# Kernel optimization log

Hardware: AMD Instinct MI355X
Metric: run time of the kernel (lower is better)

## Reference

```python
import jax, jax.numpy as jnp
import numpy as np

B, S, H = 4, 1024, 2560          # batch, seq, hidden_size
E, K, F = 32, 6, 1536            # num_experts, top_k, moe_intermediate_size
SHARED_F = 2 * 1536              # moe_num_shared_experts * moe_intermediate_size
NORM_MIN = 1e-12                 # config.moe_norm_min


def setup_inputs() -> dict:
    key = jax.random.key(0)
    ks = jax.random.split(key, 9)
    rnd = lambda k, shape, scale=0.02: jax.random.normal(k, shape, dtype=jnp.float32) * scale
    return {
        "hidden_states": jax.random.normal(ks[0], (B, S, H), dtype=jnp.float32),
        "router_w": rnd(ks[1], (E, H)),              # Ernie4_5_MoeTopKRouter.weight (fp32)
        "router_bias": jnp.zeros((E,), jnp.float32),  # moe_statics.e_score_correction_bias
        "gate_w": rnd(ks[2], (E, H, F)),
        "up_w": rnd(ks[3], (E, H, F)),
        "down_w": rnd(ks[4], (E, F, H)),
        "shared_gate_w": rnd(ks[5], (H, SHARED_F)),
        "shared_up_w": rnd(ks[6], (H, SHARED_F)),
        "shared_down_w": rnd(ks[7], (SHARED_F, H)),
    }


def _mlp(x, gw, uw, dw):
    # Ernie4_5_MoeMLP: down( silu(gate(x)) * up(x) ), no biases
    return (jax.nn.silu(x @ gw) * (x @ uw)) @ dw


def _forward(hidden_states, router_w, router_bias, gate_w, up_w, down_w,
             shared_gate_w, shared_up_w, shared_down_w):
    T = B * S
    xt = hidden_states.reshape(T, H)

    # shared experts path (always-on dense MLP)
    shared_out = _mlp(xt, shared_gate_w, shared_up_w, shared_down_w)

    # router: fp32 linear -> softmax -> (+ correction bias) -> top-k -> renorm
    logits = xt.astype(jnp.float32) @ router_w.T            # [T, E]
    probs = jax.nn.softmax(logits, axis=-1)
    top_w, top_i = jax.lax.top_k(probs + router_bias[None, :], K)  # [T, K]
    top_w = top_w / jnp.clip(jnp.sum(top_w, axis=-1, keepdims=True), NORM_MIN)
    top_w = top_w.astype(hidden_states.dtype)

    # expert combine: loop over the fixed expert set; per-token combine weight
    # cw[t] = sum_k top_w[t,k] * (top_i[t,k] == e)  (matches one-hot dispatch +
    # index_add_ scatter combine of the original)
    out = jnp.zeros_like(xt)
    for e in range(E):
        cw = jnp.sum(jnp.where(top_i == e, top_w, 0.0), axis=-1)  # [T]
        y = _mlp(xt, gate_w[e], up_w[e], down_w[e])               # [T, H]
        out = out + cw[:, None] * y

    out = out + shared_out
    return out.reshape(B, S, H)


def reference(hidden_states, router_w, router_bias, gate_w, up_w, down_w,
              shared_gate_w, shared_up_w, shared_down_w):
    return _forward(hidden_states, router_w, router_bias, gate_w, up_w, down_w,
                    shared_gate_w, shared_up_w, shared_down_w)
```

## Files before the change

kernel.cpp:

```cpp
#include <hip/hip_runtime.h>
#include <hip/hip_bf16.h>
#include <math.h>

#define T_TOK 4096
#define HID   2560
#define NEXP  32
#define KTOP  6
#define FF    1536
#define SFF   3072
#define MAXP  (T_TOK*KTOP)

typedef __attribute__((ext_vector_type(8))) short short8;
typedef __attribute__((ext_vector_type(4))) float f32x4;

static __device__ __forceinline__ unsigned short f2bf(float x){
  return __builtin_bit_cast(unsigned short, (__bf16)x);
}
static __device__ __forceinline__ float bf2f(unsigned short u){
  unsigned int x = ((unsigned int)u) << 16;
  return __builtin_bit_cast(float, x);
}

static __device__ __forceinline__ void gload_lds16(const void* g, void* l){
  __builtin_amdgcn_global_load_lds(
      (const __attribute__((address_space(1))) unsigned int*)g,
      (__attribute__((address_space(3))) unsigned int*)l, 16, 0, 0);
}

__global__ void k_cast_x(const float* __restrict__ x, unsigned short* __restrict__ xb){
  int i = (blockIdx.x * 256 + threadIdx.x) * 4;
  float4 v = *(const float4*)(x + i);
  ushort4 o;
  o.x = f2bf(v.x); o.y = f2bf(v.y); o.z = f2bf(v.z); o.w = f2bf(v.w);
  *(ushort4*)(xb + i) = o;
}

__global__ __launch_bounds__(256)
void k_transpose(const float* __restrict__ in, unsigned short* __restrict__ out,
                 const int R, const int C, const long long outBS){
  const size_t bi = (size_t)blockIdx.z * (size_t)R * C;
  const size_t bo = (size_t)blockIdx.z * (size_t)outBS;
  __shared__ unsigned short t2[64][72];
  const int r0 = blockIdx.y * 64, c0 = blockIdx.x * 64;
  const int tid = threadIdx.x;
  const int cr = tid & 15;
  const int rr = tid >> 4;
#pragma unroll
  for (int i = 0; i < 4; ++i){
    const int r = rr + 16*i;
    float4 v = *(const float4*)(in + bi + (size_t)(r0 + r)*C + c0 + cr*4);
    ushort4 p;
    p.x = f2bf(v.x); p.y = f2bf(v.y); p.z = f2bf(v.z); p.w = f2bf(v.w);
    *(ushort4*)(&t2[r][cr*4]) = p;
  }
  __syncthreads();
  const int rw = tid & 7;
  const int ro = tid >> 3;
#pragma unroll
  for (int i = 0; i < 2; ++i){
    const int c = ro + 32*i;
    ushort4 a, b;
    a.x = t2[rw*8+0][c]; a.y = t2[rw*8+1][c]; a.z = t2[rw*8+2][c]; a.w = t2[rw*8+3][c];
    b.x = t2[rw*8+4][c]; b.y = t2[rw*8+5][c]; b.z = t2[rw*8+6][c]; b.w = t2[rw*8+7][c];
    unsigned short* op = out + bo + (size_t)(c0 + c)*R + r0 + rw*8;
    *(ushort4*)(op)     = a;
    *(ushort4*)(op + 4) = b;
  }
}

__global__ void k_router(const float* __restrict__ x, const float* __restrict__ rw,
                         const float* __restrict__ rb, float* __restrict__ top_w,
                         int* __restrict__ top_i, int* __restrict__ counts){
  const int lane = threadIdx.x & 63;
  const int wv   = threadIdx.x >> 6;
  const int t    = blockIdx.x * 4 + wv;
  const float* xr = x + (size_t)t * HID;
  float xv[40];
#pragma unroll
  for (int i = 0; i < 40; ++i) xv[i] = xr[lane + 64*i];
  float sc[32];
  for (int e = 0; e < 32; ++e){
    const float* w = rw + (size_t)e * HID;
    float s = 0.f;
#pragma unroll
    for (int i = 0; i < 40; ++i) s = fmaf(xv[i], w[lane + 64*i], s);
#pragma unroll
    for (int o = 32; o; o >>= 1) s += __shfl_xor(s, o);
    sc[e] = s;
  }
  float mx = sc[0];
#pragma unroll
  for (int e = 1; e < 32; ++e) mx = fmaxf(mx, sc[e]);
  float se = 0.f;
#pragma unroll
  for (int e = 0; e < 32; ++e){ sc[e] = expf(sc[e] - mx); se += sc[e]; }
  const float inv = 1.f / se;
#pragma unroll
  for (int e = 0; e < 32; ++e) sc[e] = sc[e] * inv + rb[e];

  unsigned chosen = 0; float swv[KTOP]; int sid[KTOP]; float wsum = 0.f;
#pragma unroll
  for (int k = 0; k < KTOP; ++k){
    float bv = -1e30f; int bi = 0;
#pragma unroll
    for (int e = 0; e < 32; ++e){
      bool ok = !((chosen >> e) & 1u);
      if (ok && sc[e] > bv){ bv = sc[e]; bi = e; }
    }
    chosen |= 1u << bi; swv[k] = bv; sid[k] = bi; wsum += bv;
  }
  const float dn = fmaxf(wsum, 1e-12f);
  if (lane < KTOP){
    top_w[t*KTOP + lane] = swv[lane] / dn;
    top_i[t*KTOP + lane] = sid[lane];
    atomicAdd(counts + sid[lane], 1);
  }
}

__global__ void k_scan(const int* __restrict__ counts, int* __restrict__ offsets){
  if (threadIdx.x == 0){
    int a = 0;
    for (int e = 0; e < NEXP; ++e){ offsets[e] = a; a += counts[e]; }
    offsets[NEXP] = a;
  }
}

__global__ void k_scatter(const int* __restrict__ top_i, const float* __restrict__ top_w,
                          const int* __restrict__ offsets, int* __restrict__ cursor,
                          int* __restrict__ pair_tok, float* __restrict__ pair_w){
  const int t = blockIdx.x * 256 + threadIdx.x;
  if (t >= T_TOK) return;
#pragma unroll
  for (int k = 0; k < KTOP; ++k){
    int e = top_i[t*KTOP + k];
    int pos = offsets[e] + atomicAdd(cursor + e, 1);
    pair_tok[pos] = t;
    pair_w[pos]   = top_w[t*KTOP + k];
  }
}

template<int F8>
__global__ __launch_bounds__(256)
void k_swiglu(const unsigned short* __restrict__ y, unsigned short* __restrict__ act){
  const int i = blockIdx.x * 256 + threadIdx.x;
  const int p = i / F8, c = i % F8;
  const unsigned short* row = y + (size_t)p * (2*F8*8);
  short8 g8 = *(const short8*)(row + c*8);
  short8 u8 = *(const short8*)(row + F8*8 + c*8);
  short8 o;
#pragma unroll
  for (int j = 0; j < 8; ++j){
    float g = bf2f((unsigned short)g8[j]);
    float u = bf2f((unsigned short)u8[j]);
    float s = (g / (1.f + expf(-g))) * u;
    o[j] = (short)f2bf(s);
  }
  *(short8*)(act + (size_t)p*F8*8 + c*8) = o;
}

template<bool GROUPED, bool GATHER, int OUT>
__global__ __launch_bounds__(512, 2)
void k_gemm(const unsigned short* __restrict__ A,
            const unsigned short* __restrict__ BT,
            void* __restrict__ outp,
            const int* __restrict__ pair_tok, const float* __restrict__ pair_w,
            const int* __restrict__ counts, const int* __restrict__ offsets,
            const int N, const int K, const int ntiles)
{
  const int NH = K >> 5;
  const int total = gridDim.x;
  const int phys  = blockIdx.x;
  const int logical = (phys & 7) * (total >> 3) + (phys >> 3);
  const int mt   = logical & 15;
  const int rest = logical >> 4;
  const int n0 = (rest % ntiles) << 8;
  const int e  = rest / ntiles;

  int M, base;
  if (GROUPED){ M = counts[e]; base = offsets[e]; }
  else        { M = T_TOK;     base = 0; }
  if (mt * 256 >= M) return;
  const unsigned short* Bb = BT + (size_t)e * (size_t)N * K;

  __shared__ unsigned short AS[4*8192];
  __shared__ unsigned short BS[4*8192];

  const int tid  = threadIdx.x;
  const int lane = tid & 63;
  const int w    = tid >> 6;
  const int wr = w >> 2, wc = w & 3;

  const int lrow = lane >> 2, lchunk = lane & 3;
  const int swz = (lchunk ^ ((lrow >> 1) & 3)) * 8;
  const unsigned short *ap0, *ap1, *bp0, *bp1;
  {
    const int r0 = w*32 + lrow, r1 = w*32 + 16 + lrow;
    int i0 = min(mt*256 + r0, M - 1);
    int i1 = min(mt*256 + r1, M - 1);
    int rowA0 = GATHER ? pair_tok[base + i0] : (GROUPED ? base + i0 : i0);
    int rowA1 = GATHER ? pair_tok[base + i1] : (GROUPED ? base + i1 : i1);
    ap0 = A + (size_t)rowA0 * K + swz;
    ap1 = A + (size_t)rowA1 * K + swz;
    bp0 = Bb + (size_t)(n0 + r0) * K + swz;
    bp1 = Bb + (size_t)(n0 + r1) * K + swz;
  }

  const f32x4 zero = {0.f,0.f,0.f,0.f};
  f32x4 acc[8][4];
#pragma unroll
  for (int m = 0; m < 8; ++m)
#pragma unroll
    for (int n = 0; n < 4; ++n) acc[m][n] = zero;

  const int fr = lane & 15;
  const int fg = ((lane >> 4) ^ ((lane >> 1) & 3)) * 16;

#define STAGE_A(h)                                                          \
  { const int _s = (h) & 3; const size_t _k = (size_t)(h) * 32;             \
    gload_lds16(ap0 + _k, (char*)AS + _s*16384 + (w*32)*64);                \
    gload_lds16(ap1 + _k, (char*)AS + _s*16384 + (w*32+16)*64); }
#define STAGE_B(h)                                                          \
  { const int _s = (h) & 3; const size_t _k = (size_t)(h) * 32;             \
    gload_lds16(bp0 + _k, (char*)BS + _s*16384 + (w*32)*64);                \
    gload_lds16(bp1 + _k, (char*)BS + _s*16384 + (w*32+16)*64); }

  STAGE_A(0) STAGE_B(0) STAGE_A(1) STAGE_B(1) STAGE_A(2) STAGE_B(2)
  asm volatile("s_waitcnt vmcnt(8)" ::: "memory");
  __builtin_amdgcn_s_barrier();
  __builtin_amdgcn_sched_barrier(0);

  for (int h = 0; h < NH; ++h){
    const int s = h & 3;
    const char* _as = (const char*)AS + s*16384;
    const char* _bs = (const char*)BS + s*16384;
    short8 bq[4], af[4];
#pragma unroll
    for (int n = 0; n < 4; ++n)
      bq[n] = *(const short8*)(_bs + (wc*64 + n*16 + fr)*64 + fg);
#pragma unroll
    for (int m = 0; m < 4; ++m)
      af[m] = *(const short8*)(_as + (wr*128 + m*16 + fr)*64 + fg);
    if (h + 3 < NH) STAGE_A(h + 3)
    __builtin_amdgcn_s_barrier();
    __builtin_amdgcn_sched_barrier(0);
    __builtin_amdgcn_s_setprio(1);
#pragma unroll
    for (int m = 0; m < 4; ++m)
#pragma unroll
      for (int n = 0; n < 4; ++n)
        acc[m][n] = __builtin_amdgcn_mfma_f32_16x16x32_bf16(af[m], bq[n], acc[m][n], 0, 0, 0);
    __builtin_amdgcn_s_setprio(0);
    __builtin_amdgcn_s_barrier();
    __builtin_amdgcn_sched_barrier(0);
#pragma unroll
    for (int m = 0; m < 4; ++m)
      af[m] = *(const short8*)(_as + (wr*128 + (m+4)*16 + fr)*64 + fg);
    if (h + 3 < NH) STAGE_B(h + 3)
    __builtin_amdgcn_s_barrier();
    __builtin_amdgcn_sched_barrier(0);
    __builtin_amdgcn_s_setprio(1);
#pragma unroll
    for (int m = 0; m < 4; ++m)
#pragma unroll
      for (int n = 0; n < 4; ++n)
        acc[m+4][n] = __builtin_amdgcn_mfma_f32_16x16x32_bf16(af[m], bq[n], acc[m+4][n], 0, 0, 0);
    __builtin_amdgcn_s_setprio(0);
    if (h + 3 < NH)      asm volatile("s_waitcnt vmcnt(8)" ::: "memory");
    else if (h + 2 < NH) asm volatile("s_waitcnt vmcnt(4)" ::: "memory");
    else if (h + 1 < NH) asm volatile("s_waitcnt vmcnt(0)" ::: "memory");
    __builtin_amdgcn_s_barrier();
    __builtin_amdgcn_sched_barrier(0);
  }
#undef STAGE_A
#undef STAGE_B

#pragma unroll
  for (int m = 0; m < 8; ++m)
#pragma unroll
    for (int j = 0; j < 4; ++j){
      const int rr = mt*256 + wr*128 + m*16 + (lane >> 4)*4 + j;
      if (rr < M){
        const int col = n0 + wc*64 + (lane & 15);
        if (OUT == 0){
          unsigned short* orow = (unsigned short*)outp + (size_t)(base + rr) * N + col;
#pragma unroll
          for (int n = 0; n < 4; ++n) orow[n*16] = f2bf(acc[m][n][j]);
        } else if (OUT == 1){
          const int p = base + rr;
          const int tok = pair_tok[p];
          const float pw = pair_w[p];
          float* orow = (float*)outp + (size_t)tok * HID + col;
#pragma unroll
          for (int n = 0; n < 4; ++n) atomicAdd(orow + n*16, acc[m][n][j] * pw);
        } else {
          float* orow = (float*)outp + (size_t)rr * N + col;
#pragma unroll
          for (int n = 0; n < 4; ++n) orow[n*16] = acc[m][n][j];
        }
      }
    }
}

extern "C" void kernel_launch(void* const* d_in, const int* in_sizes, int n_in,
                              void* d_out, int out_size, void* d_ws, size_t ws_size,
                              hipStream_t stream)
{
  (void)in_sizes; (void)n_in; (void)out_size; (void)ws_size;
  const float* hid = (const float*)d_in[0];
  const float* rw  = (const float*)d_in[1];
  const float* rb  = (const float*)d_in[2];
  const float* gw  = (const float*)d_in[3];
  const float* uw  = (const float*)d_in[4];
  const float* dw  = (const float*)d_in[5];
  const float* sgw = (const float*)d_in[6];
  const float* suw = (const float*)d_in[7];
  const float* sdw = (const float*)d_in[8];
  float* out = (float*)d_out;

  char* ws = (char*)d_ws;
  size_t o = 0;
  unsigned short* xb   = (unsigned short*)(ws + o); o += (size_t)T_TOK*HID*2;
  unsigned short* act  = (unsigned short*)(ws + o); o += (size_t)MAXP*FF*2;
  unsigned short* sact = (unsigned short*)(ws + o); o += (size_t)T_TOK*SFF*2;
  unsigned short* y    = (unsigned short*)(ws + o); o += (size_t)MAXP*2*FF*2;
  unsigned short* sy   = (unsigned short*)(ws + o); o += (size_t)T_TOK*2*SFF*2;
  unsigned short* Wbuf = (unsigned short*)(ws + o);
  unsigned short* guT  = Wbuf;
  unsigned short* sguT = Wbuf + (size_t)NEXP*2*FF*HID;
  unsigned short* dT   = Wbuf;
  unsigned short* sdT  = Wbuf + (size_t)NEXP*HID*FF;
  o += (size_t)NEXP*2*FF*HID*2 + (size_t)2*SFF*HID*2;
  float* top_w    = (float*)(ws + o); o += (size_t)T_TOK*KTOP*4;
  int*   top_i    = (int*)(ws + o);   o += (size_t)T_TOK*KTOP*4;
  float* pair_w   = (float*)(ws + o); o += (size_t)MAXP*4;
  int*   pair_tok = (int*)(ws + o);   o += (size_t)MAXP*4;
  int*   counts   = (int*)(ws + o);   o += NEXP*4;
  int*   offsets  = (int*)(ws + o);   o += (NEXP+1)*4;
  int*   cursor   = (int*)(ws + o);   o += NEXP*4;

  hipMemsetAsync(counts, 0, (NEXP + (NEXP+1) + NEXP) * sizeof(int), stream);

  k_cast_x<<<(T_TOK*HID)/1024, 256, 0, stream>>>(hid, xb);
  k_router<<<T_TOK/4, 256, 0, stream>>>(hid, rw, rb, top_w, top_i, counts);
  k_scan<<<1, 64, 0, stream>>>(counts, offsets);
  k_scatter<<<T_TOK/256, 256, 0, stream>>>(top_i, top_w, offsets, cursor, pair_tok, pair_w);

  k_transpose<<<dim3(FF/64,  HID/64, NEXP), 256, 0, stream>>>(gw,  guT,                    HID, FF,  (long long)2*FF*HID);
  k_transpose<<<dim3(FF/64,  HID/64, NEXP), 256, 0, stream>>>(uw,  guT + (size_t)FF*HID,   HID, FF,  (long long)2*FF*HID);
  k_transpose<<<dim3(SFF/64, HID/64, 1),    256, 0, stream>>>(sgw, sguT,                   HID, SFF, 0);
  k_transpose<<<dim3(SFF/64, HID/64, 1),    256, 0, stream>>>(suw, sguT + (size_t)SFF*HID, HID, SFF, 0);

  k_gemm<true,  true,  0><<<16*(2*FF/256)*NEXP, 512, 0, stream>>>(
      xb, guT, y, pair_tok, nullptr, counts, offsets, 2*FF, HID, 2*FF/256);
  k_gemm<false, false, 0><<<16*(2*SFF/256), 512, 0, stream>>>(
      xb, sguT, sy, nullptr, nullptr, nullptr, nullptr, 2*SFF, HID, 2*SFF/256);
  k_swiglu<FF/8><<<(MAXP*(FF/8))/256, 256, 0, stream>>>(y, act);
  k_swiglu<SFF/8><<<(T_TOK*(SFF/8))/256, 256, 0, stream>>>(sy, sact);

  k_transpose<<<dim3(HID/64, FF/64,  NEXP), 256, 0, stream>>>(dw,  dT,  FF,  HID, (long long)HID*FF);
  k_transpose<<<dim3(HID/64, SFF/64, 1),    256, 0, stream>>>(sdw, sdT, SFF, HID, 0);

  k_gemm<false, false, 2><<<16*(HID/256), 512, 0, stream>>>(
      sact, sdT, out, nullptr, nullptr, nullptr, nullptr, HID, SFF, HID/256);
  k_gemm<true,  false, 1><<<16*(HID/256)*NEXP, 512, 0, stream>>>(
      act, dT, out, pair_tok, pair_w, counts, offsets, HID, FF, HID/256);
}
```

Before: 1.942 ms.

## Collapse two-phase GEMM main loop into single phase with one barrier

Merges the split A/B staging and the two half-tile MFMA phases into one phase per k-step. All eight A fragments are loaded up front, and only one barrier per iteration remains, with the sched_barriers removed and the loop unrolled by four. The aim is to cut barrier and synchronisation overhead and give the compiler freedom to interleave loads with MFMAs. In exchange it raises VGPR pressure through the extra fragment registers, which can lower occupancy, and it loses the explicit interleave of staging with compute.

Result: faster. 1.792 ms (-7.7%).

```diff
diff --git a/kernel.cpp b/kernel.cpp
--- a/kernel.cpp
+++ b/kernel.cpp
@@ -215,64 +215,43 @@
   const int fr = lane & 15;
   const int fg = ((lane >> 4) ^ ((lane >> 1) & 3)) * 16;
 
-#define STAGE_A(h)                                                          \
+#define STAGE(h)                                                            \
   { const int _s = (h) & 3; const size_t _k = (size_t)(h) * 32;             \
     gload_lds16(ap0 + _k, (char*)AS + _s*16384 + (w*32)*64);                \
-    gload_lds16(ap1 + _k, (char*)AS + _s*16384 + (w*32+16)*64); }
-#define STAGE_B(h)                                                          \
-  { const int _s = (h) & 3; const size_t _k = (size_t)(h) * 32;             \
+    gload_lds16(ap1 + _k, (char*)AS + _s*16384 + (w*32+16)*64);             \
     gload_lds16(bp0 + _k, (char*)BS + _s*16384 + (w*32)*64);                \
     gload_lds16(bp1 + _k, (char*)BS + _s*16384 + (w*32+16)*64); }
 
-  STAGE_A(0) STAGE_B(0) STAGE_A(1) STAGE_B(1) STAGE_A(2) STAGE_B(2)
+  STAGE(0) STAGE(1) STAGE(2)
   asm volatile("s_waitcnt vmcnt(8)" ::: "memory");
   __builtin_amdgcn_s_barrier();
-  __builtin_amdgcn_sched_barrier(0);
-
+
+#pragma unroll 4
   for (int h = 0; h < NH; ++h){
     const int s = h & 3;
     const char* _as = (const char*)AS + s*16384;
     const char* _bs = (const char*)BS + s*16384;
-    short8 bq[4], af[4];
+    short8 bq[4], af[8];
 #pragma unroll
     for (int n = 0; n < 4; ++n)
       bq[n] = *(const short8*)(_bs + (wc*64 + n*16 + fr)*64 + fg);
 #pragma unroll
-    for (int m = 0; m < 4; ++m)
+    for (int m = 0; m < 8; ++m)
       af[m] = *(const short8*)(_as + (wr*128 + m*16 + fr)*64 + fg);
-    if (h + 3 < NH) STAGE_A(h + 3)
-    __builtin_amdgcn_s_barrier();
-    __builtin_amdgcn_sched_barrier(0);
+    if (h + 3 < NH) STAGE(h + 3)
     __builtin_amdgcn_s_setprio(1);
 #pragma unroll
-    for (int m = 0; m < 4; ++m)
+    for (int m = 0; m < 8; ++m)
 #pragma unroll
       for (int n = 0; n < 4; ++n)
         acc[m][n] = __builtin_amdgcn_mfma_f32_16x16x32_bf16(af[m], bq[n], acc[m][n], 0, 0, 0);
-    __builtin_amdgcn_s_setprio(0);
-    __builtin_amdgcn_s_barrier();
-    __builtin_amdgcn_sched_barrier(0);
-#pragma unroll
-    for (int m = 0; m < 4; ++m)
-      af[m] = *(const short8*)(_as + (wr*128 + (m+4)*16 + fr)*64 + fg);
-    if (h + 3 < NH) STAGE_B(h + 3)
-    __builtin_amdgcn_s_barrier();
-    __builtin_amdgcn_sched_barrier(0);
-    __builtin_amdgcn_s_setprio(1);
-#pragma unroll
-    for (int m = 0; m < 4; ++m)
-#pragma unroll
-      for (int n = 0; n < 4; ++n)
-        acc[m+4][n] = __builtin_amdgcn_mfma_f32_16x16x32_bf16(af[m], bq[n], acc[m+4][n], 0, 0, 0);
     __builtin_amdgcn_s_setprio(0);
     if (h + 3 < NH)      asm volatile("s_waitcnt vmcnt(8)" ::: "memory");
     else if (h + 2 < NH) asm volatile("s_waitcnt vmcnt(4)" ::: "memory");
     else if (h + 1 < NH) asm volatile("s_waitcnt vmcnt(0)" ::: "memory");
     __builtin_amdgcn_s_barrier();
-    __builtin_amdgcn_sched_barrier(0);
-  }
-#undef STAGE_A
-#undef STAGE_B
+  }
+#undef STAGE
 
 #pragma unroll
   for (int m = 0; m < 8; ++m)
```
